# Optimization experiments

Measured on AMD Instinct MI355X. Metric: run time of the kernel, lower is better.

## Reference

```python
import jax, jax.numpy as jnp
import numpy as np
import math

MAX_REL = 64
NUM_HEADS = 16


def rel_pos_embeddings(table, S, max_rel):
    # distance matrix with clip_pad=True edge overrides, then lookup -> [S, S, head_dim]
    dist = jnp.arange(S)[None, :] - jnp.arange(S)[:, None]
    c = jnp.clip(dist, -max_rel, max_rel)
    c = c.at[1:-1, 0].set(-max_rel)
    c = c.at[1:-1, -1].set(max_rel)
    return table[c + max_rel]


def setup_inputs() -> dict:
    key = jax.random.key(0)
    ks = jax.random.split(key, 6)
    B, S, D = 4, 1024, 1024
    H = NUM_HEADS
    hd = D // H
    sc = 1.0 / math.sqrt(D)
    x = jax.random.normal(ks[0], (B, S, D), jnp.float32)
    mask = jax.random.randint(ks[1], (B, 1, S, S), 0, 2).astype(jnp.int32)
    qkv_w = jax.random.normal(ks[2], (3 * D, D), jnp.float32) * sc
    qkv_b = jnp.zeros((3 * D,), jnp.float32)
    o_w = jax.random.normal(ks[3], (D, D), jnp.float32) * sc
    o_b = jnp.zeros((D,), jnp.float32)
    rel_k_table = jax.random.normal(ks[4], (2 * MAX_REL + 1, hd), jnp.float32) * (1.0 / math.sqrt(hd))
    return {"x": x, "qkv_w": qkv_w, "qkv_b": qkv_b, "o_w": o_w, "o_b": o_b,
            "rel_k_table": rel_k_table, "mask": mask}


def reference(x, qkv_w, qkv_b, o_w, o_b, rel_k_table, mask):
    B, S, D = x.shape
    H = NUM_HEADS
    hd = D // H
    qkv = x @ qkv_w.T + qkv_b                      # [B, S, 3D]
    qkv = qkv.reshape(B, S, H, 3 * hd).transpose(0, 2, 1, 3)
    q, k, v = jnp.split(qkv, 3, axis=-1)           # each [B, H, S, hd]
    sk = rel_pos_embeddings(rel_k_table, S, MAX_REL)  # [S, S, hd]
    sv = sk  # original code (bug-faithfully) uses relative_position_k for both sk and sv
    logits = jnp.einsum('bhqd,bhkd->bhqk', q, k) + jnp.einsum('bhqd,qkd->bhqk', q, sk)
    logits = logits / math.sqrt(hd)
    logits = jnp.where(mask == 0, -9e15, logits)
    attn = jax.nn.softmax(logits, axis=-1)         # [B, H, S, S]
    vals = jnp.einsum('bhqk,bhkd->bhqd', attn, v) + jnp.einsum('bhqk,qkd->bhqd', attn, sv)
    vals = vals.transpose(0, 2, 1, 3).reshape(B, S, D)
    return vals @ o_w.T + o_b
```

## Files before the change

### kernel.cpp

```cpp
#include <hip/hip_runtime.h>

typedef unsigned short u16;
typedef __attribute__((ext_vector_type(8))) short bf16x8;
typedef __attribute__((ext_vector_type(4))) short u16x4;
typedef __attribute__((ext_vector_type(4))) float f32x4;

__device__ __forceinline__ u16 f2bu(float f) {
  union { float f; unsigned u; } v; v.f = f;
  unsigned r = v.u + 0x7fffu + ((v.u >> 16) & 1u);
  return (u16)(r >> 16);
}
__device__ __forceinline__ u16 f2bu_fast(float f) {
  union { float f; unsigned u; } v; v.f = f;
  return (u16)((v.u + 0x8000u) >> 16);
}
__device__ __forceinline__ float b2f(u16 s) {
  union { unsigned u; float f; } v; v.u = ((unsigned)s) << 16;
  return v.f;
}
__device__ __forceinline__ bf16x8 cvt8(float4 a, float4 b) {
  bf16x8 r;
  r[0] = (short)f2bu(a.x); r[1] = (short)f2bu(a.y);
  r[2] = (short)f2bu(a.z); r[3] = (short)f2bu(a.w);
  r[4] = (short)f2bu(b.x); r[5] = (short)f2bu(b.y);
  r[6] = (short)f2bu(b.z); r[7] = (short)f2bu(b.w);
  return r;
}
__device__ __forceinline__ f32x4 mfma16(bf16x8 a, bf16x8 b, f32x4 c) {
  return __builtin_amdgcn_mfma_f32_16x16x32_bf16(a, b, c, 0, 0, 0);
}

__global__ __launch_bounds__(256) void prep_all_k(
    const int* __restrict__ mask, unsigned long long* __restrict__ bm64,
    const float* __restrict__ x, const float* __restrict__ w,
    const float* __restrict__ o, u16* __restrict__ xb,
    u16* __restrict__ wbo, u16* __restrict__ ob,
    const float* __restrict__ tbl, u16* __restrict__ tb, u16* __restrict__ tbT) {
  int bid = blockIdx.x;
  if (bid < 16384) {
    int i = bid * 256 + threadIdx.x;
    unsigned long long bits = __ballot(mask[i] != 0);
    if ((threadIdx.x & 63) == 0) bm64[i >> 6] = bits;
  } else if (bid < 20480) {
    int cb = bid - 16384;
    const float* src; u16* dst; int off;
    if (cb < 2048)      { src = x; dst = xb;  off = cb * 2048; }
    else if (cb < 3584) { src = w; dst = wbo; off = (cb - 2048) * 2048; }
    else                { src = o; dst = ob;  off = (cb - 3584) * 2048; }
    int idx = off + threadIdx.x * 8;
    float4 a = *(const float4*)(src + idx);
    float4 b = *(const float4*)(src + idx + 4);
    *(bf16x8*)(dst + idx) = cvt8(a, b);
  } else {
    int idx = (bid - 20480) * 256 + threadIdx.x;
    int r = idx >> 6, d = idx & 63;
    float v = (r < 129) ? tbl[r * 64 + d] : 0.f;
    u16 bv = f2bu(v);
    tb[r * 64 + d] = bv;
    tbT[d * 160 + r] = bv;
  }
}

__global__ __launch_bounds__(256) void gemm_qkv_k(
    const u16* __restrict__ A, const u16* __restrict__ Bw,
    const float* __restrict__ bias,
    u16* __restrict__ qb, u16* __restrict__ kb, u16* __restrict__ vt) {
  __shared__ u16 As[128][40];
  __shared__ u16 Bs[128][40];
  const int tid = threadIdx.x;
  const int l = tid & 63, w = tid >> 6;
  const int wr = w >> 1, wc = w & 1;
  const int fr = l & 15, kq = (l >> 4) * 8;
  const int bid = blockIdx.x;
  const int xcd = bid & 7;
  const int jx = bid >> 3;
  const int nG = jx / 48;
  const int jj = jx % 48;
  const int tm = (xcd * 4 + jj / 12) * 128;
  const int tn = (nG * 12 + jj % 12) * 128;
  const int sr = tid >> 1, sc = (tid & 1) * 16;
  const u16* Ag = A + (size_t)(tm + sr) * 1024 + sc;
  const u16* Bg = Bw + (size_t)(tn + sr) * 1024 + sc;
  f32x4 acc[4][4] = {};
  auto compute = [&]() {
    bf16x8 af[4], bfv[4];
#pragma unroll
    for (int mi = 0; mi < 4; ++mi) af[mi] = *(const bf16x8*)&As[wr * 64 + mi * 16 + fr][kq];
#pragma unroll
    for (int ni = 0; ni < 4; ++ni) bfv[ni] = *(const bf16x8*)&Bs[wc * 64 + ni * 16 + fr][kq];
#pragma unroll
    for (int mi = 0; mi < 4; ++mi)
#pragma unroll
      for (int ni = 0; ni < 4; ++ni)
        acc[mi][ni] = mfma16(af[mi], bfv[ni], acc[mi][ni]);
  };
  bf16x8 aX0, aX1, bX0, bX1, aY0, aY1, bY0, bY1;
  aX0 = *(const bf16x8*)(Ag);     aX1 = *(const bf16x8*)(Ag + 8);
  bX0 = *(const bf16x8*)(Bg);     bX1 = *(const bf16x8*)(Bg + 8);
#pragma unroll 1
  for (int kt = 0; kt < 32; kt += 2) {
    aY0 = *(const bf16x8*)(Ag + (kt + 1) * 32);
    aY1 = *(const bf16x8*)(Ag + (kt + 1) * 32 + 8);
    bY0 = *(const bf16x8*)(Bg + (kt + 1) * 32);
    bY1 = *(const bf16x8*)(Bg + (kt + 1) * 32 + 8);
    __syncthreads();
    *(bf16x8*)&As[sr][sc] = aX0; *(bf16x8*)&As[sr][sc + 8] = aX1;
    *(bf16x8*)&Bs[sr][sc] = bX0; *(bf16x8*)&Bs[sr][sc + 8] = bX1;
    __syncthreads();
    compute();
    __syncthreads();
    if (kt + 2 < 32) {
      aX0 = *(const bf16x8*)(Ag + (kt + 2) * 32);
      aX1 = *(const bf16x8*)(Ag + (kt + 2) * 32 + 8);
      bX0 = *(const bf16x8*)(Bg + (kt + 2) * 32);
      bX1 = *(const bf16x8*)(Bg + (kt + 2) * 32 + 8);
    }
    *(bf16x8*)&As[sr][sc] = aY0; *(bf16x8*)&As[sr][sc + 8] = aY1;
    *(bf16x8*)&Bs[sr][sc] = bY0; *(bf16x8*)&Bs[sr][sc + 8] = bY1;
    __syncthreads();
    compute();
  }
#pragma unroll
  for (int mi = 0; mi < 4; ++mi)
#pragma unroll
    for (int ni = 0; ni < 4; ++ni)
#pragma unroll
      for (int j = 0; j < 4; ++j) {
        int gm = tm + wr * 64 + mi * 16 + (l >> 4) * 4 + j;
        int gn = tn + wc * 64 + ni * 16 + fr;
        float v = acc[mi][ni][j] + bias[gn];
        int b = gm >> 10, s = gm & 1023;
        unsigned gnu = (unsigned)gn;
        unsigned h = gnu / 192u;
        unsigned rem = gnu - h * 192u;
        unsigned which = rem >> 6, d = rem & 63u;
        int bh = b * 16 + (int)h;
        u16 bv = f2bu(v);
        if (which == 0u)      qb[((size_t)bh * 1024 + s) * 64 + d] = bv;
        else if (which == 1u) kb[((size_t)bh * 1024 + s) * 64 + d] = bv;
        else                  vt[((size_t)bh * 64 + d) * 1024 + s] = bv;
      }
}

#define QRS 132
__global__ __launch_bounds__(256) void attn_k(
    const u16* __restrict__ qb, const u16* __restrict__ kb,
    const u16* __restrict__ vt, const u16* __restrict__ tb,
    const u16* __restrict__ tbT, const unsigned long long* __restrict__ bm64,
    u16* __restrict__ vals) {
  __shared__ u16 Kbuf[64 * 64];
  __shared__ u16 Vbuf[64 * 64];
  __shared__ u16 qrs[64 * QRS];
  const int tid = threadIdx.x;
  const int l = tid & 63, w = tid >> 6;
  const int fr = l & 15, g = l >> 4, kq = g * 8, g4 = g * 4;
  const int blk = ((int)blockIdx.x & 7) * 128 + ((int)blockIdx.x >> 3);
  const int qt = blk & 15, bh = blk >> 4;
  const int b = bh >> 4, h = bh & 15;
  const int qbase = qt * 64 + w * 16;
  const int q = qbase + fr;
  const u16* kbase = kb + (size_t)bh * 65536;
  const u16* vbase = vt + (size_t)bh * 65536;
  const int srow0 = tid >> 3, sslot = tid & 7;
  const int p5 = (sslot >> 2) & 1, p4 = (sslot >> 1) & 1, p3 = sslot & 1;
  const int vb0 = p5 * 32 + p3 * 16 + p4 * 4;
  bf16x8 sK0, sK1, sV0, sV1;
  auto ldStage = [&](int c) {
    const u16* ks = kbase + (size_t)(c * 64) * 64;
    sK0 = *(const bf16x8*)(ks + srow0 * 64 + sslot * 8);
    sK1 = *(const bf16x8*)(ks + (srow0 + 32) * 64 + sslot * 8);
    const u16* vs = vbase + c * 64 + sslot * 8;
    sV0 = *(const bf16x8*)(vs + (size_t)srow0 * 1024);
    sV1 = *(const bf16x8*)(vs + (size_t)(srow0 + 32) * 1024);
  };
  auto wrV = [&](int d, bf16x8 v) {
    int s0 = vb0 >> 3, sub = vb0 & 7;
    int a0 = d * 64 + ((s0 ^ (d & 7)) * 8 + sub);
    int a1 = d * 64 + (((s0 + 1) ^ (d & 7)) * 8 + sub);
    u16x4 lo = {v[0], v[1], v[2], v[3]};
    u16x4 hi = {v[4], v[5], v[6], v[7]};
    *(u16x4*)&Vbuf[a0] = lo;
    *(u16x4*)&Vbuf[a1] = hi;
  };
  auto wrStage = [&]() {
    *(bf16x8*)&Kbuf[srow0 * 64 + (sslot ^ (srow0 & 7)) * 8] = sK0;
    *(bf16x8*)&Kbuf[(srow0 + 32) * 64 + (sslot ^ ((srow0 + 32) & 7)) * 8] = sK1;
    wrV(srow0, sV0);
    wrV(srow0 + 32, sV1);
  };
  ldStage(0);
  const u16* qrow = qb + ((size_t)bh * 1024 + qbase) * 64;
  bf16x8 qa0 = *(const bf16x8*)(qrow + fr * 64 + kq);
  bf16x8 qa1 = *(const bf16x8*)(qrow + fr * 64 + 32 + kq);
  f32x4 a_t0 = {}, a_t8 = {};
#pragma unroll
  for (int t = 0; t < 9; ++t) {
    const u16* tp = tb + (t * 16 + fr) * 64 + kq;
    bf16x8 t0 = *(const bf16x8*)(tp);
    bf16x8 t1 = *(const bf16x8*)(tp + 32);
    f32x4 a = {0.f, 0.f, 0.f, 0.f};
    a = mfma16(t0, qa0, a);
    a = mfma16(t1, qa1, a);
#pragma unroll
    for (int j = 0; j < 4; ++j) {
      int rg = t * 16 + g4 + j;
      if (rg < 129) qrs[(w * 16 + fr) * QRS + rg] = f2bu(a[j]);
    }
    if (t == 0) a_t0 = a;
    if (t == 8) a_t8 = a;
  }
  const float q0r = __shfl(a_t0[0], fr);
  const float q128r = __shfl(a_t8[0], fr);
  u16* qpl = qrs + (w * 16 + fr) * QRS;
  if (g == 0) {
    int loEnd = (q == 0) ? 63 : (q <= 63 ? 64 - q : 0);
    for (int r = 1; r <= loEnd; ++r) qpl[r] = 0;
    int hiStart = (q >= 960 && q <= 1022) ? (1087 - q) : (q == 1023 ? 65 : 128);
    for (int r = hiStart; r <= 127; ++r) qpl[r] = 0;
  }
  const unsigned* bmp = (const unsigned*)(bm64 + (((size_t)b << 10) + q) * 16);
  unsigned bmLoX = bmp[0], bmHiX = bmp[1], bmLoY = 0, bmHiY = 0;
  const float C1 = 0.18033688011112042f;
  const float C2 = 17.31234049066756f;
  float ps = 0.f, psA = 0.f, psB = 0.f;
  f32x4 acc[4] = {};
  auto kfrag = [&](int t2, int hh) -> bf16x8 {
    int rk = t2 * 16 + fr;
    int sl = (g + 4 * hh) ^ (rk & 7);
    return *(const bf16x8*)&Kbuf[rk * 64 + sl * 8];
  };
  auto vfrag = [&](int dg, int hh) -> bf16x8 {
    int d = dg * 16 + fr;
    int sl = (hh * 4 + g) ^ (d & 7);
    return *(const bf16x8*)&Vbuf[d * 64 + sl * 8];
  };
#pragma unroll 1
  for (int c = 0; c < 16; ++c) {
    __syncthreads();
    wrStage();
    __syncthreads();
    __builtin_amdgcn_s_setprio(1);
    if (c < 15) {
      ldStage(c + 1);
      bmLoY = bmp[(c + 1) * 2];
      bmHiY = bmp[(c + 1) * 2 + 1];
    }
    bf16x8 pa0, pa1;
#pragma unroll
    for (int t2 = 0; t2 < 4; ++t2) {
      f32x4 a = {0.f, 0.f, 0.f, 0.f};
      a = mfma16(kfrag(t2, 0), qa0, a);
      a = mfma16(kfrag(t2, 1), qa1, a);
      int ncol = c * 64 + t2 * 16;
      unsigned wsel = (t2 < 2) ? bmLoX : bmHiX;
      if (ncol + 79 <= qbase) {
#pragma unroll
        for (int j = 0; j < 4; ++j) {
          float s = a[j] + q0r;
          unsigned bit = (wsel >> (g4 + ((t2 & 1) * 16 + j))) & 1u;
          float arg = bit ? __builtin_fmaf(s, C1, -C2) : -1e30f;
          float e = __builtin_amdgcn_exp2f(arg);
          ps += e; psA += e;
          u16 pv = f2bu_fast(e);
          if (t2 < 2) pa0[t2 * 4 + j] = (short)pv; else pa1[(t2 - 2) * 4 + j] = (short)pv;
        }
      } else if (ncol >= qbase + 79) {
#pragma unroll
        for (int j = 0; j < 4; ++j) {
          float s = a[j] + q128r;
          unsigned bit = (wsel >> (g4 + ((t2 & 1) * 16 + j))) & 1u;
          float arg = bit ? __builtin_fmaf(s, C1, -C2) : -1e30f;
          float e = __builtin_amdgcn_exp2f(arg);
          ps += e; psB += e;
          u16 pv = f2bu_fast(e);
          if (t2 < 2) pa0[t2 * 4 + j] = (short)pv; else pa1[(t2 - 2) * 4 + j] = (short)pv;
        }
      } else {
#pragma unroll
        for (int j = 0; j < 4; ++j) {
          int kgl = ncol + g4 + j;
          int dd = kgl - q;
          int rdx = dd < -64 ? 0 : (dd > 64 ? 128 : dd + 64);
          bool ov = (q >= 1 && q <= 1022);
          bool edge = ov && (kgl == 0 || kgl == 1023);
          if (edge) rdx = (kgl == 0) ? 0 : 128;
          float s = a[j] + b2f(qpl[rdx]);
          unsigned bit = (wsel >> (g4 + ((t2 & 1) * 16 + j))) & 1u;
          float arg = bit ? __builtin_fmaf(s, C1, -C2) : -1e30f;
          float e = __builtin_amdgcn_exp2f(arg);
          ps += e;
          psA += (rdx == 0) ? e : 0.f;
          psB += (rdx == 128) ? e : 0.f;
          u16 pv = f2bu_fast(e);
          if (t2 < 2) pa0[t2 * 4 + j] = (short)pv; else pa1[(t2 - 2) * 4 + j] = (short)pv;
          int r = dd + 64;
          if (r >= 1 && r <= 127 && !edge) qpl[r] = pv;
        }
      }
    }
#pragma unroll
    for (int dg = 0; dg < 4; ++dg) {
      acc[dg] = mfma16(pa0, vfrag(dg, 0), acc[dg]);
      acc[dg] = mfma16(pa1, vfrag(dg, 1), acc[dg]);
    }
    __builtin_amdgcn_s_setprio(0);
    bmLoX = bmLoY; bmHiX = bmHiY;
  }
  if (g == 0) qpl[0] = 0;
#pragma unroll
  for (int off = 16; off <= 32; off <<= 1) {
    ps += __shfl_xor(ps, off);
    psA += __shfl_xor(psA, off);
    psB += __shfl_xor(psB, off);
  }
  float psO[4], psAO[4], psBO[4];
#pragma unroll
  for (int j = 0; j < 4; ++j) {
    psO[j] = __shfl(ps, g4 + j);
    psAO[j] = __shfl(psA, g4 + j);
    psBO[j] = __shfl(psB, g4 + j);
  }
  const u16* srow = qrs + (w * 16 + fr) * QRS + kq;
  bf16x8 sa0 = *(const bf16x8*)(srow);
  bf16x8 sa1 = *(const bf16x8*)(srow + 32);
  bf16x8 sa2 = *(const bf16x8*)(srow + 64);
  bf16x8 sa3 = *(const bf16x8*)(srow + 96);
#pragma unroll
  for (int dg = 0; dg < 4; ++dg) {
    int dc = dg * 16 + fr;
    const u16* tq = tbT + dc * 160 + kq;
    f32x4 av = acc[dg];
    av = mfma16(sa0, *(const bf16x8*)(tq), av);
    av = mfma16(sa1, *(const bf16x8*)(tq + 32), av);
    av = mfma16(sa2, *(const bf16x8*)(tq + 64), av);
    av = mfma16(sa3, *(const bf16x8*)(tq + 96), av);
    float t0v = b2f(tb[dc]);
    float t128v = b2f(tb[128 * 64 + dc]);
#pragma unroll
    for (int j = 0; j < 4; ++j) {
      float val = (av[j] + psAO[j] * t0v + psBO[j] * t128v) / psO[j];
      int sg = qbase + g4 + j;
      vals[((size_t)b * 1024 + sg) * 1024 + h * 64 + dc] = f2bu(val);
    }
  }
}

__global__ __launch_bounds__(256) void gemm_out_k(
    const u16* __restrict__ A, const u16* __restrict__ Bw,
    const float* __restrict__ bias, float* __restrict__ out) {
  __shared__ u16 As[128][40];
  __shared__ u16 Bs[128][40];
  const int tid = threadIdx.x;
  const int l = tid & 63, w = tid >> 6;
  const int wr = w >> 1, wc = w & 1;
  const int fr = l & 15, kq = (l >> 4) * 8;
  const int bid = blockIdx.x;
  const int xcd = bid & 7;
  const int jx = bid >> 3;
  const int tm = (xcd * 4 + (jx >> 3)) * 128;
  const int tn = (jx & 7) * 128;
  const int sr = tid >> 1, sc = (tid & 1) * 16;
  const u16* Ag = A + (size_t)(tm + sr) * 1024 + sc;
  const u16* Bg = Bw + (size_t)(tn + sr) * 1024 + sc;
  f32x4 acc[4][4] = {};
  auto compute = [&]() {
    bf16x8 af[4], bfv[4];
#pragma unroll
    for (int mi = 0; mi < 4; ++mi) af[mi] = *(const bf16x8*)&As[wr * 64 + mi * 16 + fr][kq];
#pragma unroll
    for (int ni = 0; ni < 4; ++ni) bfv[ni] = *(const bf16x8*)&Bs[wc * 64 + ni * 16 + fr][kq];
#pragma unroll
    for (int mi = 0; mi < 4; ++mi)
#pragma unroll
      for (int ni = 0; ni < 4; ++ni)
        acc[mi][ni] = mfma16(af[mi], bfv[ni], acc[mi][ni]);
  };
  bf16x8 aX0, aX1, bX0, bX1, aY0, aY1, bY0, bY1;
  aX0 = *(const bf16x8*)(Ag);     aX1 = *(const bf16x8*)(Ag + 8);
  bX0 = *(const bf16x8*)(Bg);     bX1 = *(const bf16x8*)(Bg + 8);
#pragma unroll 1
  for (int kt = 0; kt < 32; kt += 2) {
    aY0 = *(const bf16x8*)(Ag + (kt + 1) * 32);
    aY1 = *(const bf16x8*)(Ag + (kt + 1) * 32 + 8);
    bY0 = *(const bf16x8*)(Bg + (kt + 1) * 32);
    bY1 = *(const bf16x8*)(Bg + (kt + 1) * 32 + 8);
    __syncthreads();
    *(bf16x8*)&As[sr][sc] = aX0; *(bf16x8*)&As[sr][sc + 8] = aX1;
    *(bf16x8*)&Bs[sr][sc] = bX0; *(bf16x8*)&Bs[sr][sc + 8] = bX1;
    __syncthreads();
    compute();
    __syncthreads();
    if (kt + 2 < 32) {
      aX0 = *(const bf16x8*)(Ag + (kt + 2) * 32);
      aX1 = *(const bf16x8*)(Ag + (kt + 2) * 32 + 8);
      bX0 = *(const bf16x8*)(Bg + (kt + 2) * 32);
      bX1 = *(const bf16x8*)(Bg + (kt + 2) * 32 + 8);
    }
    *(bf16x8*)&As[sr][sc] = aY0; *(bf16x8*)&As[sr][sc + 8] = aY1;
    *(bf16x8*)&Bs[sr][sc] = bY0; *(bf16x8*)&Bs[sr][sc + 8] = bY1;
    __syncthreads();
    compute();
  }
#pragma unroll
  for (int mi = 0; mi < 4; ++mi)
#pragma unroll
    for (int ni = 0; ni < 4; ++ni)
#pragma unroll
      for (int j = 0; j < 4; ++j) {
        int gm = tm + wr * 64 + mi * 16 + (l >> 4) * 4 + j;
        int gn = tn + wc * 64 + ni * 16 + fr;
        out[(size_t)gm * 1024 + gn] = acc[mi][ni][j] + bias[gn];
      }
}

extern "C" void kernel_launch(void* const* d_in, const int* in_sizes, int n_in,
                              void* d_out, int out_size, void* d_ws, size_t ws_size,
                              hipStream_t stream) {
  (void)in_sizes; (void)n_in; (void)out_size; (void)ws_size;
  const float* x    = (const float*)d_in[0];
  const float* qkvw = (const float*)d_in[1];
  const float* qkvb = (const float*)d_in[2];
  const float* ow   = (const float*)d_in[3];
  const float* ob   = (const float*)d_in[4];
  const float* tbl  = (const float*)d_in[5];
  const int*   mask = (const int*)d_in[6];
  float* out = (float*)d_out;
  char* ws = (char*)d_ws;
  u16* tb   = (u16*)(ws);
  u16* tbT  = (u16*)(ws + 20480);
  u16* qb   = (u16*)(ws + 40960);
  u16* kb   = (u16*)(ws + 40960 + 8388608ull);
  u16* vt   = (u16*)(ws + 40960 + 2ull * 8388608ull);
  u16* xbvals = (u16*)(ws + 40960 + 3ull * 8388608ull);
  unsigned long long* bm64 = (unsigned long long*)(ws + 40960 + 4ull * 8388608ull);
  u16* wb   = (u16*)(ws + 40960 + 4ull * 8388608ull + 524288ull);
  u16* owb  = (u16*)(ws + 40960 + 4ull * 8388608ull + 524288ull + 6291456ull);

  prep_all_k<<<dim3(20520), dim3(256), 0, stream>>>(mask, bm64, x, qkvw, ow,
                                                    xbvals, wb, owb, tbl, tb, tbT);
  gemm_qkv_k<<<dim3(768), dim3(256), 0, stream>>>(xbvals, wb, qkvb, qb, kb, vt);
  attn_k<<<dim3(1024), dim3(256), 0, stream>>>(qb, kb, vt, tb, tbT, bm64, xbvals);
  gemm_out_k<<<dim3(256), dim3(256), 0, stream>>>(xbvals, owb, ob, out);
}
```

Before: 158.6 us.

## Double-buffer LDS in projection GEMMs and drop XCD-aware tile mapping

Both projection GEMMs move from a single LDS tile with two-register prefetch and two barriers per k-step to a double-buffered LDS ring. Each k-step now has one barrier, and the next tile's global load is issued right after that barrier. The XCD-aware block-to-tile swizzle is replaced with a plain row-major mapping, which can change L2 locality across chiplets. LDS use per block doubles, which may lower occupancy.

New measurement: 132.6 us. 16.4% less time.

```diff
diff --git a/kernel.cpp b/kernel.cpp
--- a/kernel.cpp
+++ b/kernel.cpp
@@ -65,60 +65,43 @@
     const u16* __restrict__ A, const u16* __restrict__ Bw,
     const float* __restrict__ bias,
     u16* __restrict__ qb, u16* __restrict__ kb, u16* __restrict__ vt) {
-  __shared__ u16 As[128][40];
-  __shared__ u16 Bs[128][40];
+  __shared__ u16 As[2][128][40];
+  __shared__ u16 Bs[2][128][40];
   const int tid = threadIdx.x;
   const int l = tid & 63, w = tid >> 6;
   const int wr = w >> 1, wc = w & 1;
   const int fr = l & 15, kq = (l >> 4) * 8;
   const int bid = blockIdx.x;
-  const int xcd = bid & 7;
-  const int jx = bid >> 3;
-  const int nG = jx / 48;
-  const int jj = jx % 48;
-  const int tm = (xcd * 4 + jj / 12) * 128;
-  const int tn = (nG * 12 + jj % 12) * 128;
+  const int tn = (bid % 24) * 128, tm = (bid / 24) * 128;
   const int sr = tid >> 1, sc = (tid & 1) * 16;
   const u16* Ag = A + (size_t)(tm + sr) * 1024 + sc;
   const u16* Bg = Bw + (size_t)(tn + sr) * 1024 + sc;
   f32x4 acc[4][4] = {};
-  auto compute = [&]() {
+  bf16x8 a0, a1, b0, b1;
+  a0 = *(const bf16x8*)(Ag);      a1 = *(const bf16x8*)(Ag + 8);
+  b0 = *(const bf16x8*)(Bg);      b1 = *(const bf16x8*)(Bg + 8);
+#pragma unroll 1
+  for (int kt = 0; kt < 32; ++kt) {
+    const int db = kt & 1;
+    *(bf16x8*)&As[db][sr][sc] = a0; *(bf16x8*)&As[db][sr][sc + 8] = a1;
+    *(bf16x8*)&Bs[db][sr][sc] = b0; *(bf16x8*)&Bs[db][sr][sc + 8] = b1;
+    __syncthreads();
+    if (kt < 31) {
+      a0 = *(const bf16x8*)(Ag + (kt + 1) * 32);
+      a1 = *(const bf16x8*)(Ag + (kt + 1) * 32 + 8);
+      b0 = *(const bf16x8*)(Bg + (kt + 1) * 32);
+      b1 = *(const bf16x8*)(Bg + (kt + 1) * 32 + 8);
+    }
     bf16x8 af[4], bfv[4];
 #pragma unroll
-    for (int mi = 0; mi < 4; ++mi) af[mi] = *(const bf16x8*)&As[wr * 64 + mi * 16 + fr][kq];
-#pragma unroll
-    for (int ni = 0; ni < 4; ++ni) bfv[ni] = *(const bf16x8*)&Bs[wc * 64 + ni * 16 + fr][kq];
+    for (int mi = 0; mi < 4; ++mi) af[mi] = *(const bf16x8*)&As[db][wr * 64 + mi * 16 + fr][kq];
+#pragma unroll
+    for (int ni = 0; ni < 4; ++ni) bfv[ni] = *(const bf16x8*)&Bs[db][wc * 64 + ni * 16 + fr][kq];
 #pragma unroll
     for (int mi = 0; mi < 4; ++mi)
 #pragma unroll
       for (int ni = 0; ni < 4; ++ni)
         acc[mi][ni] = mfma16(af[mi], bfv[ni], acc[mi][ni]);
-  };
-  bf16x8 aX0, aX1, bX0, bX1, aY0, aY1, bY0, bY1;
-  aX0 = *(const bf16x8*)(Ag);     aX1 = *(const bf16x8*)(Ag + 8);
-  bX0 = *(const bf16x8*)(Bg);     bX1 = *(const bf16x8*)(Bg + 8);
-#pragma unroll 1
-  for (int kt = 0; kt < 32; kt += 2) {
-    aY0 = *(const bf16x8*)(Ag + (kt + 1) * 32);
-    aY1 = *(const bf16x8*)(Ag + (kt + 1) * 32 + 8);
-    bY0 = *(const bf16x8*)(Bg + (kt + 1) * 32);
-    bY1 = *(const bf16x8*)(Bg + (kt + 1) * 32 + 8);
-    __syncthreads();
-    *(bf16x8*)&As[sr][sc] = aX0; *(bf16x8*)&As[sr][sc + 8] = aX1;
-    *(bf16x8*)&Bs[sr][sc] = bX0; *(bf16x8*)&Bs[sr][sc + 8] = bX1;
-    __syncthreads();
-    compute();
-    __syncthreads();
-    if (kt + 2 < 32) {
-      aX0 = *(const bf16x8*)(Ag + (kt + 2) * 32);
-      aX1 = *(const bf16x8*)(Ag + (kt + 2) * 32 + 8);
-      bX0 = *(const bf16x8*)(Bg + (kt + 2) * 32);
-      bX1 = *(const bf16x8*)(Bg + (kt + 2) * 32 + 8);
-    }
-    *(bf16x8*)&As[sr][sc] = aY0; *(bf16x8*)&As[sr][sc + 8] = aY1;
-    *(bf16x8*)&Bs[sr][sc] = bY0; *(bf16x8*)&Bs[sr][sc + 8] = bY1;
-    __syncthreads();
-    compute();
   }
 #pragma unroll
   for (int mi = 0; mi < 4; ++mi)
@@ -348,58 +331,43 @@
 __global__ __launch_bounds__(256) void gemm_out_k(
     const u16* __restrict__ A, const u16* __restrict__ Bw,
     const float* __restrict__ bias, float* __restrict__ out) {
-  __shared__ u16 As[128][40];
-  __shared__ u16 Bs[128][40];
+  __shared__ u16 As[2][128][40];
+  __shared__ u16 Bs[2][128][40];
   const int tid = threadIdx.x;
   const int l = tid & 63, w = tid >> 6;
   const int wr = w >> 1, wc = w & 1;
   const int fr = l & 15, kq = (l >> 4) * 8;
   const int bid = blockIdx.x;
-  const int xcd = bid & 7;
-  const int jx = bid >> 3;
-  const int tm = (xcd * 4 + (jx >> 3)) * 128;
-  const int tn = (jx & 7) * 128;
+  const int tn = (bid % 8) * 128, tm = (bid / 8) * 128;
   const int sr = tid >> 1, sc = (tid & 1) * 16;
   const u16* Ag = A + (size_t)(tm + sr) * 1024 + sc;
   const u16* Bg = Bw + (size_t)(tn + sr) * 1024 + sc;
   f32x4 acc[4][4] = {};
-  auto compute = [&]() {
+  bf16x8 a0, a1, b0, b1;
+  a0 = *(const bf16x8*)(Ag);      a1 = *(const bf16x8*)(Ag + 8);
+  b0 = *(const bf16x8*)(Bg);      b1 = *(const bf16x8*)(Bg + 8);
+#pragma unroll 1
+  for (int kt = 0; kt < 32; ++kt) {
+    const int db = kt & 1;
+    *(bf16x8*)&As[db][sr][sc] = a0; *(bf16x8*)&As[db][sr][sc + 8] = a1;
+    *(bf16x8*)&Bs[db][sr][sc] = b0; *(bf16x8*)&Bs[db][sr][sc + 8] = b1;
+    __syncthreads();
+    if (kt < 31) {
+      a0 = *(const bf16x8*)(Ag + (kt + 1) * 32);
+      a1 = *(const bf16x8*)(Ag + (kt + 1) * 32 + 8);
+      b0 = *(const bf16x8*)(Bg + (kt + 1) * 32);
+      b1 = *(const bf16x8*)(Bg + (kt + 1) * 32 + 8);
+    }
     bf16x8 af[4], bfv[4];
 #pragma unroll
-    for (int mi = 0; mi < 4; ++mi) af[mi] = *(const bf16x8*)&As[wr * 64 + mi * 16 + fr][kq];
-#pragma unroll
-    for (int ni = 0; ni < 4; ++ni) bfv[ni] = *(const bf16x8*)&Bs[wc * 64 + ni * 16 + fr][kq];
+    for (int mi = 0; mi < 4; ++mi) af[mi] = *(const bf16x8*)&As[db][wr * 64 + mi * 16 + fr][kq];
+#pragma unroll
+    for (int ni = 0; ni < 4; ++ni) bfv[ni] = *(const bf16x8*)&Bs[db][wc * 64 + ni * 16 + fr][kq];
 #pragma unroll
     for (int mi = 0; mi < 4; ++mi)
 #pragma unroll
       for (int ni = 0; ni < 4; ++ni)
         acc[mi][ni] = mfma16(af[mi], bfv[ni], acc[mi][ni]);
-  };
-  bf16x8 aX0, aX1, bX0, bX1, aY0, aY1, bY0, bY1;
-  aX0 = *(const bf16x8*)(Ag);     aX1 = *(const bf16x8*)(Ag + 8);
-  bX0 = *(const bf16x8*)(Bg);     bX1 = *(const bf16x8*)(Bg + 8);
-#pragma unroll 1
-  for (int kt = 0; kt < 32; kt += 2) {
-    aY0 = *(const bf16x8*)(Ag + (kt + 1) * 32);
-    aY1 = *(const bf16x8*)(Ag + (kt + 1) * 32 + 8);
-    bY0 = *(const bf16x8*)(Bg + (kt + 1) * 32);
-    bY1 = *(const bf16x8*)(Bg + (kt + 1) * 32 + 8);
-    __syncthreads();
-    *(bf16x8*)&As[sr][sc] = aX0; *(bf16x8*)&As[sr][sc + 8] = aX1;
-    *(bf16x8*)&Bs[sr][sc] = bX0; *(bf16x8*)&Bs[sr][sc + 8] = bX1;
-    __syncthreads();
-    compute();
-    __syncthreads();
-    if (kt + 2 < 32) {
-      aX0 = *(const bf16x8*)(Ag + (kt + 2) * 32);
-      aX1 = *(const bf16x8*)(Ag + (kt + 2) * 32 + 8);
-      bX0 = *(const bf16x8*)(Bg + (kt + 2) * 32);
-      bX1 = *(const bf16x8*)(Bg + (kt + 2) * 32 + 8);
-    }
-    *(bf16x8*)&As[sr][sc] = aY0; *(bf16x8*)&As[sr][sc + 8] = aY1;
-    *(bf16x8*)&Bs[sr][sc] = bY0; *(bf16x8*)&Bs[sr][sc + 8] = bY1;
-    __syncthreads();
-    compute();
   }
 #pragma unroll
   for (int mi = 0; mi < 4; ++mi)
```
